# Kernel optimization log

Measured on AMD Instinct MI355X. Metric: run time of the kernel, lower is better.

## Reference

```python
import jax, jax.numpy as jnp
import numpy as np

NUM_TREES = 256
MAX_TREE_DEPTH = 10
NUM_NODES = 2 ** (MAX_TREE_DEPTH + 1) - 1  # 2047, complete binary tree
N_FEATURES = 256
N_CLASSES = 8
BATCH = 32768


def setup_inputs() -> dict:
    key = jax.random.key(0)
    kx, kf, kt, kv = jax.random.split(key, 4)
    x = jax.random.normal(kx, (BATCH, N_FEATURES), dtype=jnp.float32)

    # Complete binary tree: internal node i has children 2i+1 / 2i+2; leaves self-loop
    # (matches hummingbird's padding where leaf left==right==self, so extra depth
    #  iterations are no-ops). lefts/rights are stored as float32, as in the module.
    node = np.arange(NUM_NODES)
    n_internal = (NUM_NODES - 1) // 2
    left1 = np.where(node < n_internal, 2 * node + 1, node).astype(np.float32)
    right1 = np.where(node < n_internal, 2 * node + 2, node).astype(np.float32)
    lefts = jnp.asarray(np.tile(left1, NUM_TREES))            # [T*N]
    rights = jnp.asarray(np.tile(right1, NUM_TREES))          # [T*N]

    features = jax.random.randint(kf, (NUM_TREES * NUM_NODES,), 0, N_FEATURES, dtype=jnp.int32)
    thresholds = jax.random.normal(kt, (NUM_TREES * NUM_NODES,), dtype=jnp.float32)
    values = jax.random.normal(kv, (NUM_TREES * NUM_NODES, N_CLASSES), dtype=jnp.float32)
    nodes_offset = jnp.arange(NUM_TREES, dtype=jnp.int32) * NUM_NODES  # [T]
    return {"x": x, "lefts": lefts, "rights": rights, "features": features,
            "thresholds": thresholds, "values": values, "nodes_offset": nodes_offset}


def reference(x, lefts, rights, features, thresholds, values, nodes_offset):
    B = x.shape[0]
    T = nodes_offset.shape[0]
    # flat global node index per (sample, tree), start at each tree's root
    idx = jnp.broadcast_to(nodes_offset[None, :], (B, T)).reshape(-1)  # [B*T]
    for _ in range(MAX_TREE_DEPTH):
        feat = features[idx].reshape(B, T)                     # [B,T] feature id per tree
        fv = jnp.take_along_axis(x, feat, axis=1)              # [B,T] feature value
        thr = thresholds[idx].reshape(B, T)
        l = lefts[idx].reshape(B, T)
        r = rights[idx].reshape(B, T)
        nxt = jnp.where(fv >= thr, r, l).astype(jnp.int32)     # local child index
        idx = (nxt + nodes_offset[None, :]).reshape(-1)        # back to global flat index
    return values[idx].reshape(B, T, values.shape[-1])         # [B, T, n_classes]
```

## Files before the change

### kernel.cpp

```cpp
#include <hip/hip_runtime.h>
#include <stdint.h>


#define T_TREES   256
#define NNODES    2047
#define NFEAT     256
#define NCLASS    8
#define DEPTH     10
#define BATCH     32768

#define SPB       64
#define THREADS   512
#define ILP       8
#define TPB       ((THREADS / 64) * ILP)
#define TGROUPS   (T_TREES / TPB)

__global__ void pack_tf_kernel(const float* __restrict__ thr,
                               const int*   __restrict__ feat,
                               float2*      __restrict__ tf, int n) {
  int i = blockIdx.x * blockDim.x + threadIdx.x;
  if (i < n) tf[i] = make_float2(thr[i], __int_as_float(feat[i]));
}

template <bool PACKED>
__global__ __launch_bounds__(THREADS)
void forest_kernel(const float* __restrict__ x,
                   const int*   __restrict__ features,
                   const float* __restrict__ thresholds,
                   const float2* __restrict__ tf,
                   const float* __restrict__ values,
                   float*       __restrict__ out) {
  __shared__ float xs[SPB * NFEAT];

  const int tid = threadIdx.x;
  const int tg    = blockIdx.x % TGROUPS;
  const int chunk = blockIdx.x / TGROUPS;
  const int b0    = chunk * SPB;

  for (int i = tid; i < SPB * NFEAT; i += THREADS) {
    int row = i >> 8;
    int col = i & 255;
    xs[(row << 8) | (col ^ (row & 31))] = x[(size_t)(b0 + row) * NFEAT + col];
  }
  __syncthreads();

  const int w  = tid >> 6;
  const int l  = tid & 63;
  const int sw = l & 31;
  const float* xrow = xs + (l << 8);
  float* outb = out + (size_t)(b0 + l) * (T_TREES * NCLASS);

  const int tbase = tg * TPB + w * ILP;

  int node[ILP];
#pragma unroll
  for (int k = 0; k < ILP; ++k) node[k] = 0;

#pragma unroll
  for (int d = 0; d < DEPTH; ++d) {
    float tv[ILP];
    int   fi[ILP];
#pragma unroll
    for (int k = 0; k < ILP; ++k) {
      const size_t idx = (size_t)(tbase + k) * NNODES + node[k];
      if (PACKED) {
        float2 a = tf[idx];
        tv[k] = a.x;
        fi[k] = __float_as_int(a.y);
      } else {
        tv[k] = thresholds[idx];
        fi[k] = features[idx];
      }
    }
    float fv[ILP];
#pragma unroll
    for (int k = 0; k < ILP; ++k) fv[k] = xrow[fi[k] ^ sw];
#pragma unroll
    for (int k = 0; k < ILP; ++k)
      node[k] = 2 * node[k] + 1 + (fv[k] >= tv[k] ? 1 : 0);
  }

#pragma unroll
  for (int k = 0; k < ILP; ++k) {
    const int t = tbase + k;
    const float4* vp =
        (const float4*)(values + ((size_t)t * NNODES + node[k]) * NCLASS);
    float4 v0 = vp[0];
    float4 v1 = vp[1];
    float4* op = (float4*)(outb + t * NCLASS);
    op[0] = v0;
    op[1] = v1;
  }
}

extern "C" void kernel_launch(void* const* d_in, const int* in_sizes, int n_in,
                              void* d_out, int out_size, void* d_ws,
                              size_t ws_size, hipStream_t stream) {
  const float* x          = (const float*)d_in[0];
  const int*   features   = (const int*)d_in[3];
  const float* thresholds = (const float*)d_in[4];
  const float* values     = (const float*)d_in[5];
  float* out = (float*)d_out;

  const int n_nodes_total = T_TREES * NNODES;
  const size_t packed_bytes = (size_t)n_nodes_total * sizeof(float2);

  const int grid = (BATCH / SPB) * TGROUPS;

  if (ws_size >= packed_bytes) {
    float2* tf = (float2*)d_ws;
    pack_tf_kernel<<<(n_nodes_total + 255) / 256, 256, 0, stream>>>(
        thresholds, features, tf, n_nodes_total);
    forest_kernel<true><<<grid, THREADS, 0, stream>>>(
        x, features, thresholds, tf, values, out);
  } else {
    forest_kernel<false><<<grid, THREADS, 0, stream>>>(
        x, features, thresholds, (const float2*)nullptr, values, out);
  }
}
```

Measured before the change: 447.5 us.

## Stage leaf outputs through shared memory for coalesced stores; vectorize x loads

The x tile is now loaded with float4 global reads instead of scalar reads. The output write is restructured so leaf values are first written into the shared-memory tile (reused, XOR-swizzled), then each half of the samples is written out with fully coalesced float4 stores across the block. Previously each lane wrote 32 bytes per tree at strided sample rows. The cost is extra barriers, two serialized passes, and half the lanes idle during each staging phase.

```diff
diff --git a/kernel.cpp b/kernel.cpp
--- a/kernel.cpp
+++ b/kernel.cpp
@@ -37,10 +37,17 @@
   const int chunk = blockIdx.x / TGROUPS;
   const int b0    = chunk * SPB;
 
-  for (int i = tid; i < SPB * NFEAT; i += THREADS) {
-    int row = i >> 8;
-    int col = i & 255;
-    xs[(row << 8) | (col ^ (row & 31))] = x[(size_t)(b0 + row) * NFEAT + col];
+  for (int i = tid; i < SPB * NFEAT / 4; i += THREADS) {
+    const int row = i >> 6;
+    const int c4  = i & 63;
+    const float4 v =
+        ((const float4*)x)[(size_t)(b0 + row) * (NFEAT / 4) + c4];
+    const int base = row << 8;
+    const int s    = row & 31;
+    xs[base | ((4 * c4 + 0) ^ s)] = v.x;
+    xs[base | ((4 * c4 + 1) ^ s)] = v.y;
+    xs[base | ((4 * c4 + 2) ^ s)] = v.z;
+    xs[base | ((4 * c4 + 3) ^ s)] = v.w;
   }
   __syncthreads();
 
@@ -48,7 +55,6 @@
   const int l  = tid & 63;
   const int sw = l & 31;
   const float* xrow = xs + (l << 8);
-  float* outb = out + (size_t)(b0 + l) * (T_TREES * NCLASS);
 
   const int tbase = tg * TPB + w * ILP;
 
@@ -80,16 +86,38 @@
       node[k] = 2 * node[k] + 1 + (fv[k] >= tv[k] ? 1 : 0);
   }
 
+  __syncthreads();
+  const int half = l >> 5;
+  const int r    = l & 31;
+
 #pragma unroll
-  for (int k = 0; k < ILP; ++k) {
-    const int t = tbase + k;
-    const float4* vp =
-        (const float4*)(values + ((size_t)t * NNODES + node[k]) * NCLASS);
-    float4 v0 = vp[0];
-    float4 v1 = vp[1];
-    float4* op = (float4*)(outb + t * NCLASS);
-    op[0] = v0;
-    op[1] = v1;
+  for (int p = 0; p < 2; ++p) {
+    if (half == p) {
+      const int key = (r & 7) << 2;
+#pragma unroll
+      for (int k = 0; k < ILP; ++k) {
+        const int t = tbase + k;
+        const float4* vp =
+            (const float4*)(values + ((size_t)t * NNODES + node[k]) * NCLASS);
+        const float4 v0 = vp[0];
+        const float4 v1 = vp[1];
+        const int c0 = (w * ILP + k) * NCLASS;
+        *(float4*)&xs[r * 512 + ((c0    ) ^ key)] = v0;
+        *(float4*)&xs[r * 512 + ((c0 + 4) ^ key)] = v1;
+      }
+    }
+    __syncthreads();
+#pragma unroll
+    for (int j = 0; j < 8; ++j) {
+      const int f4   = j * THREADS + tid;
+      const int row  = f4 >> 7;
+      const int colf = (f4 & 127) << 2;
+      const float4 v =
+          *(const float4*)&xs[row * 512 + (colf ^ ((row & 7) << 2))];
+      *(float4*)&out[(size_t)(b0 + p * 32 + row) * (T_TREES * NCLASS) +
+                     tg * (TPB * NCLASS) + colf] = v;
+    }
+    __syncthreads();
   }
 }
 
```

Result: faster. 396.0 us (-11.5%).
